# Performance work log

Measured on AMD Instinct MI355X. Metric: run time of the kernel, lower is better.

## Reference

```python
import jax, jax.numpy as jnp
import numpy as np

N = 2048
K = 10000
MEAN = 1.0
CHUNK = 8  # rows per scan step; intermediate is CHUNK x N x K (~655 MB)


def setup_inputs() -> dict:
    key = jax.random.key(0)
    # torch.rand(N, 10000) * mean / 2
    W = jax.random.uniform(key, (N, K), dtype=jnp.float32) * (MEAN / 2.0)
    return {"W": W}


def reference(W):
    # H[i, j] = max_k ( |W[i,k]| + |W[j,k]| )  -- tropical (max-plus) gram matrix
    A = jnp.abs(W)                     # (N, K)
    n, k = A.shape
    chunks = A.reshape(n // CHUNK, CHUNK, k)

    @jax.checkpoint
    def body(carry, a):                # a: (CHUNK, K)
        # (CHUNK, N, K) broadcast-add, max-reduce over K -> (CHUNK, N)
        h = jnp.max(a[:, None, :] + A[None, :, :], axis=-1)
        return carry, h

    _, H = jax.lax.scan(body, None, chunks)  # (n//CHUNK, CHUNK, N)
    return H.reshape(n, n)
```

## Files before the change

### kernel.cpp

```cpp
#include <hip/hip_runtime.h>
#include <math.h>


constexpr int N  = 2048;
constexpr int K  = 10000;
constexpr int BT = 128;
constexpr int BK = 32;
constexpr int NT = N / BT;
constexpr int NTRI = NT * (NT + 1) / 2;
constexpr int TILES8 = 72;
constexpr int BID8 = TILES8 * 8;
constexpr int CH8 = 1252;
constexpr int CH7 = 1432;
constexpr int NS8 = 40;
constexpr int NS7 = 45;

__device__ __forceinline__ float max3f(float a, float b, float c) {
    float d;
    asm("v_max3_f32 %0, %1, %2, %3" : "=v"(d) : "v"(a), "v"(b), "v"(c));
    return d;
}

__global__ void zero_out_kernel(float4* __restrict__ p, int n4) {
    const int i = blockIdx.x * blockDim.x + threadIdx.x;
    if (i < n4) p[i] = make_float4(0.f, 0.f, 0.f, 0.f);
}

__global__ __launch_bounds__(256, 2)
void tropical_gram_kernel(const float* __restrict__ W, float* __restrict__ H) {
    __shared__ float As[BK][BT];
    __shared__ float Bs[BK][BT];

    const int tid = threadIdx.x;

    const int bid = blockIdx.x;
    int tile, q, kbeg, nstep;
    if (bid < BID8) {
        tile  = bid >> 3;
        q     = bid & 7;
        kbeg  = q * CH8;
        nstep = NS8;
    } else {
        const int r = bid - BID8;
        tile  = TILES8 + r / 7;
        q     = r % 7;
        kbeg  = q * CH7;
        nstep = NS7;
    }
    int t = tile;
    int bi = 0;
    while (t >= NT - bi) { t -= NT - bi; ++bi; }
    const int bj = bi + t;
    const int i0 = bi * BT, j0 = bj * BT;
    const bool diag = (bi == bj);

    const int srow = tid & 127;
    const int kh   = tid >> 7;
    const float* rowi = W + (size_t)(i0 + srow) * K + kbeg + kh * 16;
    const float* rowj = W + (size_t)(j0 + srow) * K + kbeg + kh * 16;

    const int tx = tid & 15, ty = tid >> 4;
    const int ra = ty * 4, rb = ra + 64;
    const int ca = tx * 4, cb = ca + 64;

    float acc[8][8];
#pragma unroll
    for (int m = 0; m < 8; ++m)
#pragma unroll
        for (int n = 0; n < 8; ++n) acc[m][n] = 0.0f;

    float4 va[4], vb[4];
    const float4 z4 = make_float4(0.f, 0.f, 0.f, 0.f);

    auto fetchA = [&](int s) {
#pragma unroll
        for (int qq = 0; qq < 4; ++qq) {
            const int kg = kbeg + kh * 16 + s * BK + qq * 4;
            va[qq] = (kg < K) ? *reinterpret_cast<const float4*>(rowi + s * BK + qq * 4) : z4;
        }
    };
    auto fetchB = [&](int s) {
#pragma unroll
        for (int qq = 0; qq < 4; ++qq) {
            const int kg = kbeg + kh * 16 + s * BK + qq * 4;
            vb[qq] = (kg < K) ? *reinterpret_cast<const float4*>(rowj + s * BK + qq * 4) : z4;
        }
    };

    fetchA(0);
    if (!diag) fetchB(0);

    const float (*Bsrc)[BT] = diag ? As : Bs;

    for (int s = 0; s < nstep; ++s) {
        __syncthreads();
#pragma unroll
        for (int qq = 0; qq < 4; ++qq) {
            const int kb = kh * 16 + qq * 4;
            As[kb + 0][srow] = fabsf(va[qq].x);
            As[kb + 1][srow] = fabsf(va[qq].y);
            As[kb + 2][srow] = fabsf(va[qq].z);
            As[kb + 3][srow] = fabsf(va[qq].w);
        }
        if (!diag) {
#pragma unroll
            for (int qq = 0; qq < 4; ++qq) {
                const int kb = kh * 16 + qq * 4;
                Bs[kb + 0][srow] = fabsf(vb[qq].x);
                Bs[kb + 1][srow] = fabsf(vb[qq].y);
                Bs[kb + 2][srow] = fabsf(vb[qq].z);
                Bs[kb + 3][srow] = fabsf(vb[qq].w);
            }
        }
        if (s + 1 < nstep) {
            fetchA(s + 1);
            if (!diag) fetchB(s + 1);
        }
        __syncthreads();

#pragma unroll 2
        for (int kk = 0; kk < BK; kk += 2) {
            const float4 A0a = *reinterpret_cast<const float4*>(&As[kk][ra]);
            const float4 A0b = *reinterpret_cast<const float4*>(&As[kk][rb]);
            const float4 A1a = *reinterpret_cast<const float4*>(&As[kk + 1][ra]);
            const float4 A1b = *reinterpret_cast<const float4*>(&As[kk + 1][rb]);
            const float4 B0a = *reinterpret_cast<const float4*>(&Bsrc[kk][ca]);
            const float4 B0b = *reinterpret_cast<const float4*>(&Bsrc[kk][cb]);
            const float4 B1a = *reinterpret_cast<const float4*>(&Bsrc[kk + 1][ca]);
            const float4 B1b = *reinterpret_cast<const float4*>(&Bsrc[kk + 1][cb]);
            const float a0[8] = {A0a.x, A0a.y, A0a.z, A0a.w, A0b.x, A0b.y, A0b.z, A0b.w};
            const float a1[8] = {A1a.x, A1a.y, A1a.z, A1a.w, A1b.x, A1b.y, A1b.z, A1b.w};
            const float b0[8] = {B0a.x, B0a.y, B0a.z, B0a.w, B0b.x, B0b.y, B0b.z, B0b.w};
            const float b1[8] = {B1a.x, B1a.y, B1a.z, B1a.w, B1b.x, B1b.y, B1b.z, B1b.w};
#pragma unroll
            for (int m = 0; m < 8; ++m) {
#pragma unroll
                for (int n = 0; n < 8; ++n) {
                    const float t0 = a0[m] + b0[n];
                    const float t1 = a1[m] + b1[n];
                    acc[m][n] = max3f(acc[m][n], t0, t1);
                }
            }
        }
    }

    int* Hi = (int*)H;
#pragma unroll
    for (int m = 0; m < 8; ++m) {
        const int r = (m < 4) ? (ra + m) : (rb + m - 4);
#pragma unroll
        for (int n = 0; n < 8; ++n) {
            const int c = (n < 4) ? (ca + n) : (cb + n - 4);
            atomicMax(&Hi[(size_t)(i0 + r) * N + j0 + c], __float_as_int(acc[m][n]));
        }
    }
}

constexpr int MT  = 64;
constexpr int NT64 = N / MT;
constexpr int NMIR = NT64 * (NT64 - 1) / 2;

__global__ __launch_bounds__(256)
void mirror_kernel(float* __restrict__ H) {
    __shared__ float S[MT][MT + 1];
    int t = blockIdx.x;
    int ti = 0;
    while (t >= NT64 - 1 - ti) { t -= NT64 - 1 - ti; ++ti; }
    const int tj = ti + 1 + t;
    const int r0 = ti * MT, c0 = tj * MT;
    const int tid = threadIdx.x;
#pragma unroll
    for (int w = 0; w < 16; ++w) {
        const int idx = w * 256 + tid;
        const int r = idx >> 6, c = idx & 63;
        S[r][c] = H[(size_t)(r0 + r) * N + c0 + c];
    }
    __syncthreads();
#pragma unroll
    for (int w = 0; w < 16; ++w) {
        const int idx = w * 256 + tid;
        const int r = idx >> 6, c = idx & 63;
        H[(size_t)(c0 + r) * N + r0 + c] = S[c][r];
    }
}

extern "C" void kernel_launch(void* const* d_in, const int* in_sizes, int n_in,
                              void* d_out, int out_size, void* d_ws, size_t ws_size,
                              hipStream_t stream) {
    const float* W = (const float*)d_in[0];
    float* H = (float*)d_out;
    (void)in_sizes; (void)n_in; (void)d_ws; (void)ws_size; (void)out_size;

    const int n4 = N * N / 4;
    zero_out_kernel<<<(n4 + 255) / 256, 256, 0, stream>>>((float4*)H, n4);
    tropical_gram_kernel<<<dim3(1024), dim3(256), 0, stream>>>(W, H);
    mirror_kernel<<<dim3(NMIR), dim3(256), 0, stream>>>(H);
}
```

Measured before the change: 985.0 us.

## Pre-transpose |W| into workspace and stream B operand from global registers

Adds a kernel that writes a transposed, absolute-valued copy of W (K x N) into the workspace, so the gram kernel can load k-major rows with coalesced float4 loads and no per-tile abs or transpose. The new gram kernel keeps only the A tile in shared memory and loads the B operand straight from global/L2 into double-buffered registers, which halves LDS traffic and allows 3 blocks per CU. It also uses two-wide vector adds that the compiler may turn into packed fp32 ops. The cost is an extra pass over W of about 80 MB, many more global loads issued from inside the inner loop, and higher register pressure. The old kernel stays as a fallback when the workspace is too small.

```diff
diff --git a/kernel.cpp b/kernel.cpp
--- a/kernel.cpp
+++ b/kernel.cpp
@@ -14,6 +14,9 @@
 constexpr int CH7 = 1432;
 constexpr int NS8 = 40;
 constexpr int NS7 = 45;
+constexpr size_t WT_BYTES = (size_t)K * N * sizeof(float);
+
+typedef float f32x2 __attribute__((ext_vector_type(2)));
 
 __device__ __forceinline__ float max3f(float a, float b, float c) {
     float d;
@@ -26,25 +29,43 @@
     if (i < n4) p[i] = make_float4(0.f, 0.f, 0.f, 0.f);
 }
 
-__global__ __launch_bounds__(256, 2)
-void tropical_gram_kernel(const float* __restrict__ W, float* __restrict__ H) {
+__global__ __launch_bounds__(256)
+void transpose_abs_kernel(const float* __restrict__ W, float* __restrict__ WT) {
+    __shared__ float S[64][65];
+    const int i0 = blockIdx.x * 64;
+    const int k0 = blockIdx.y * 64;
+    const int tid = threadIdx.x;
+#pragma unroll
+    for (int w = 0; w < 16; ++w) {
+        const int idx = w * 256 + tid;
+        const int r = idx >> 6, c = idx & 63;
+        if (k0 + c < K) S[r][c] = fabsf(W[(size_t)(i0 + r) * K + k0 + c]);
+    }
+    __syncthreads();
+#pragma unroll
+    for (int w = 0; w < 16; ++w) {
+        const int idx = w * 256 + tid;
+        const int r = idx >> 6, c = idx & 63;
+        if (k0 + r < K) WT[(size_t)(k0 + r) * N + i0 + c] = S[c][r];
+    }
+}
+
+__global__ __launch_bounds__(256, 3)
+void gram_wt_kernel(const float* __restrict__ WT, float* __restrict__ H) {
     __shared__ float As[BK][BT];
-    __shared__ float Bs[BK][BT];
 
     const int tid = threadIdx.x;
 
     const int bid = blockIdx.x;
-    int tile, q, kbeg, nstep;
+    int tile, kbeg, nstep;
     if (bid < BID8) {
         tile  = bid >> 3;
-        q     = bid & 7;
-        kbeg  = q * CH8;
+        kbeg  = (bid & 7) * CH8;
         nstep = NS8;
     } else {
         const int r = bid - BID8;
         tile  = TILES8 + r / 7;
-        q     = r % 7;
-        kbeg  = q * CH7;
+        kbeg  = (r % 7) * CH7;
         nstep = NS7;
     }
     int t = tile;
@@ -52,12 +73,9 @@
     while (t >= NT - bi) { t -= NT - bi; ++bi; }
     const int bj = bi + t;
     const int i0 = bi * BT, j0 = bj * BT;
-    const bool diag = (bi == bj);
-
-    const int srow = tid & 127;
-    const int kh   = tid >> 7;
-    const float* rowi = W + (size_t)(i0 + srow) * K + kbeg + kh * 16;
-    const float* rowj = W + (size_t)(j0 + srow) * K + kbeg + kh * 16;
+
+    const int skk  = tid >> 3;
+    const int soff = (tid & 7) * 16;
 
     const int tx = tid & 15, ty = tid >> 4;
     const int ra = ty * 4, rb = ra + 64;
@@ -69,9 +87,107 @@
 #pragma unroll
         for (int n = 0; n < 8; ++n) acc[m][n] = 0.0f;
 
+    float4 va[4];
+    auto fetchA = [&](int s) {
+        int kg = kbeg + s * BK + skk;
+        if (kg > K - 1) kg = K - 1;
+        const float* src = WT + (size_t)kg * N + i0 + soff;
+#pragma unroll
+        for (int q = 0; q < 4; ++q)
+            va[q] = *reinterpret_cast<const float4*>(src + q * 4);
+    };
+
+    const float* bAp = WT + j0 + ca;
+    const float* bBp = WT + j0 + cb;
+    float4 b[2][4];
+    auto fetchB = [&](int buf, int kg) {
+        int k0c = kg     > K - 1 ? K - 1 : kg;
+        int k1c = kg + 1 > K - 1 ? K - 1 : kg + 1;
+        b[buf][0] = *reinterpret_cast<const float4*>(bAp + (size_t)k0c * N);
+        b[buf][1] = *reinterpret_cast<const float4*>(bBp + (size_t)k0c * N);
+        b[buf][2] = *reinterpret_cast<const float4*>(bAp + (size_t)k1c * N);
+        b[buf][3] = *reinterpret_cast<const float4*>(bBp + (size_t)k1c * N);
+    };
+
+    fetchA(0);
+    fetchB(0, kbeg);
+
+    for (int s = 0; s < nstep; ++s) {
+        __syncthreads();
+#pragma unroll
+        for (int q = 0; q < 4; ++q)
+            *reinterpret_cast<float4*>(&As[skk][soff + q * 4]) = va[q];
+        if (s + 1 < nstep) fetchA(s + 1);
+        __syncthreads();
+
+        const int kgs = kbeg + s * BK;
+#pragma unroll
+        for (int p = 0; p < 16; ++p) {
+            fetchB((p + 1) & 1, kgs + 2 * p + 2);
+            const int kk = 2 * p;
+            const float4 A0a = *reinterpret_cast<const float4*>(&As[kk][ra]);
+            const float4 A0b = *reinterpret_cast<const float4*>(&As[kk][rb]);
+            const float4 A1a = *reinterpret_cast<const float4*>(&As[kk + 1][ra]);
+            const float4 A1b = *reinterpret_cast<const float4*>(&As[kk + 1][rb]);
+            const float a0[8] = {A0a.x, A0a.y, A0a.z, A0a.w, A0b.x, A0b.y, A0b.z, A0b.w};
+            const float a1[8] = {A1a.x, A1a.y, A1a.z, A1a.w, A1b.x, A1b.y, A1b.z, A1b.w};
+            const float4 c0 = b[p & 1][0], c1 = b[p & 1][1];
+            const float4 c2 = b[p & 1][2], c3 = b[p & 1][3];
+            const f32x2 b0[4] = {{c0.x, c0.y}, {c0.z, c0.w}, {c1.x, c1.y}, {c1.z, c1.w}};
+            const f32x2 b1[4] = {{c2.x, c2.y}, {c2.z, c2.w}, {c3.x, c3.y}, {c3.z, c3.w}};
+#pragma unroll
+            for (int m = 0; m < 8; ++m) {
+                const f32x2 am0 = {a0[m], a0[m]};
+                const f32x2 am1 = {a1[m], a1[m]};
+#pragma unroll
+                for (int np = 0; np < 4; ++np) {
+                    const f32x2 t0 = am0 + b0[np];
+                    const f32x2 t1 = am1 + b1[np];
+                    acc[m][2 * np]     = max3f(acc[m][2 * np],     t0.x, t1.x);
+                    acc[m][2 * np + 1] = max3f(acc[m][2 * np + 1], t0.y, t1.y);
+                }
+            }
+        }
+    }
+
+    int* Hi = (int*)H;
+#pragma unroll
+    for (int m = 0; m < 8; ++m) {
+        const int r = (m < 4) ? (ra + m) : (rb + m - 4);
+#pragma unroll
+        for (int n = 0; n < 8; ++n) {
+            const int c = (n < 4) ? (ca + n) : (cb + n - 4);
+            atomicMax(&Hi[(size_t)(i0 + r) * N + j0 + c], __float_as_int(acc[m][n]));
+        }
+    }
+}
+
+__global__ __launch_bounds__(256, 2)
+void tropical_gram_kernel(const float* __restrict__ W, float* __restrict__ H) {
+    __shared__ float As[BK][BT];
+    __shared__ float Bs[BK][BT];
+    const int tid = threadIdx.x;
+    const int bid = blockIdx.x;
+    int tile, kbeg, nstep;
+    if (bid < BID8) { tile = bid >> 3; kbeg = (bid & 7) * CH8; nstep = NS8; }
+    else { const int r = bid - BID8; tile = TILES8 + r / 7; kbeg = (r % 7) * CH7; nstep = NS7; }
+    int t = tile; int bi = 0;
+    while (t >= NT - bi) { t -= NT - bi; ++bi; }
+    const int bj = bi + t;
+    const int i0 = bi * BT, j0 = bj * BT;
+    const bool diag = (bi == bj);
+    const int srow = tid & 127, kh = tid >> 7;
+    const float* rowi = W + (size_t)(i0 + srow) * K + kbeg + kh * 16;
+    const float* rowj = W + (size_t)(j0 + srow) * K + kbeg + kh * 16;
+    const int tx = tid & 15, ty = tid >> 4;
+    const int ra = ty * 4, rb = ra + 64, ca = tx * 4, cb = ca + 64;
+    float acc[8][8];
+#pragma unroll
+    for (int m = 0; m < 8; ++m)
+#pragma unroll
+        for (int n = 0; n < 8; ++n) acc[m][n] = 0.0f;
     float4 va[4], vb[4];
     const float4 z4 = make_float4(0.f, 0.f, 0.f, 0.f);
-
     auto fetchA = [&](int s) {
 #pragma unroll
         for (int qq = 0; qq < 4; ++qq) {
@@ -86,12 +202,9 @@
             vb[qq] = (kg < K) ? *reinterpret_cast<const float4*>(rowj + s * BK + qq * 4) : z4;
         }
     };
-
     fetchA(0);
     if (!diag) fetchB(0);
-
     const float (*Bsrc)[BT] = diag ? As : Bs;
-
     for (int s = 0; s < nstep; ++s) {
         __syncthreads();
 #pragma unroll
@@ -112,12 +225,8 @@
                 Bs[kb + 3][srow] = fabsf(vb[qq].w);
             }
         }
-        if (s + 1 < nstep) {
-            fetchA(s + 1);
-            if (!diag) fetchB(s + 1);
-        }
+        if (s + 1 < nstep) { fetchA(s + 1); if (!diag) fetchB(s + 1); }
         __syncthreads();
-
 #pragma unroll 2
         for (int kk = 0; kk < BK; kk += 2) {
             const float4 A0a = *reinterpret_cast<const float4*>(&As[kk][ra]);
@@ -133,17 +242,12 @@
             const float b0[8] = {B0a.x, B0a.y, B0a.z, B0a.w, B0b.x, B0b.y, B0b.z, B0b.w};
             const float b1[8] = {B1a.x, B1a.y, B1a.z, B1a.w, B1b.x, B1b.y, B1b.z, B1b.w};
 #pragma unroll
-            for (int m = 0; m < 8; ++m) {
-#pragma unroll
-                for (int n = 0; n < 8; ++n) {
-                    const float t0 = a0[m] + b0[n];
-                    const float t1 = a1[m] + b1[n];
-                    acc[m][n] = max3f(acc[m][n], t0, t1);
-                }
-            }
-        }
-    }
-
+            for (int m = 0; m < 8; ++m)
+#pragma unroll
+                for (int n = 0; n < 8; ++n)
+                    acc[m][n] = max3f(acc[m][n], a0[m] + b0[n], a1[m] + b1[n]);
+        }
+    }
     int* Hi = (int*)H;
 #pragma unroll
     for (int m = 0; m < 8; ++m) {
@@ -156,7 +260,7 @@
     }
 }
 
-constexpr int MT  = 64;
+constexpr int MT = 64;
 constexpr int NT64 = N / MT;
 constexpr int NMIR = NT64 * (NT64 - 1) / 2;
 
@@ -189,10 +293,17 @@
                               hipStream_t stream) {
     const float* W = (const float*)d_in[0];
     float* H = (float*)d_out;
-    (void)in_sizes; (void)n_in; (void)d_ws; (void)ws_size; (void)out_size;
+    (void)in_sizes; (void)n_in; (void)out_size;
 
     const int n4 = N * N / 4;
     zero_out_kernel<<<(n4 + 255) / 256, 256, 0, stream>>>((float4*)H, n4);
-    tropical_gram_kernel<<<dim3(1024), dim3(256), 0, stream>>>(W, H);
+
+    if (ws_size >= WT_BYTES) {
+        float* WT = (float*)d_ws;
+        transpose_abs_kernel<<<dim3(N / 64, (K + 63) / 64), dim3(256), 0, stream>>>(W, WT);
+        gram_wt_kernel<<<dim3(1024), dim3(256), 0, stream>>>(WT, H);
+    } else {
+        tropical_gram_kernel<<<dim3(1024), dim3(256), 0, stream>>>(W, H);
+    }
     mirror_kernel<<<dim3(NMIR), dim3(256), 0, stream>>>(H);
 }
```

Measured after the change: 1.022 ms. 3.7% more time.
